# Optimization experiments

Hardware: AMD Instinct MI355X
Metric: run time of the kernel (lower is better)

Reference implementation:

```python
import jax, jax.numpy as jnp
import numpy as np

B, H, W, C = 2, 64, 64, 192
DM = int(2.0 * C)   # d_inner = ssm_ratio * hidden_dim = 384
N = 16              # d_state
R = 12              # dt_rank = ceil(C / 16)
K = 4               # scan directions


def _ln(x, g, b, eps):
    mu = jnp.mean(x, axis=-1, keepdims=True)
    var = jnp.var(x, axis=-1, keepdims=True)
    return (x - mu) * jax.lax.rsqrt(var + eps) * g + b


def setup_inputs() -> dict:
    key = jax.random.key(0)
    ks = jax.random.split(key, 8)
    return {
        "input": jax.random.normal(ks[0], (B, H, W, C), jnp.float32),
        "norm_g": jnp.ones((C,), jnp.float32),
        "norm_b": jnp.zeros((C,), jnp.float32),
        "in_proj_w": jax.random.normal(ks[1], (C, 2 * DM), jnp.float32) * 0.02,
        "conv_w": jax.random.normal(ks[2], (DM, 1, 3, 3), jnp.float32) * 0.1,
        "conv_b": jnp.zeros((DM,), jnp.float32),
        "x_proj_w": jax.random.normal(ks[3], (K, R + 2 * N, DM), jnp.float32) * 0.02,
        "dt_w": jax.random.normal(ks[4], (K, DM, R), jnp.float32) * 0.1,
        "dt_b": jax.random.uniform(ks[5], (K, DM), jnp.float32, -4.0, -2.0),
        "A_logs": jnp.tile(jnp.log(jnp.arange(1, N + 1, dtype=jnp.float32))[None, None, :], (K, DM, 1)),
        "Ds": jnp.ones((K, DM), jnp.float32),
        "out_norm_g": jnp.ones((DM,), jnp.float32),
        "out_norm_b": jnp.zeros((DM,), jnp.float32),
        "out_proj_w": jax.random.normal(ks[6], (DM, C), jnp.float32) * 0.02,
    }


def _selective_scan(us, deltas, A, Bs, Cs):
    # us, deltas: (B,K,D,L); A: (K,D,N); Bs, Cs: (B,K,N,L)
    u_l = jnp.moveaxis(us, -1, 0)       # (L,B,K,D)
    d_l = jnp.moveaxis(deltas, -1, 0)   # (L,B,K,D)
    B_l = jnp.moveaxis(Bs, -1, 0)       # (L,B,K,N)
    C_l = jnp.moveaxis(Cs, -1, 0)       # (L,B,K,N)
    h0 = jnp.zeros(us.shape[:3] + (A.shape[-1],), us.dtype)  # (B,K,D,N)

    def step(h, xs):
        u_t, d_t, b_t, c_t = xs
        dA = jnp.exp(d_t[..., None] * A)                       # (B,K,D,N)
        h = dA * h + (d_t * u_t)[..., None] * b_t[:, :, None, :]
        y = jnp.einsum('bkdn,bkn->bkd', h, c_t)
        return h, y

    _, ys = jax.lax.scan(step, h0, (u_l, d_l, B_l, C_l))
    return jnp.moveaxis(ys, 0, -1)  # (B,K,D,L)


def reference(input, norm_g, norm_b, in_proj_w, conv_w, conv_b, x_proj_w,
              dt_w, dt_b, A_logs, Ds, out_norm_g, out_norm_b, out_proj_w):
    Bz, Hh, Ww, Cc = input.shape
    L = Hh * Ww
    # pre-norm
    xn = _ln(input, norm_g, norm_b, 1e-6)
    # input projection -> x, z
    xz = xn @ in_proj_w                      # (B,H,W,2*DM)
    x, z = jnp.split(xz, 2, axis=-1)
    # depthwise conv + SiLU (channels-first)
    x = jnp.transpose(x, (0, 3, 1, 2))       # (B,DM,H,W)
    Dm = x.shape[1]
    x = jax.lax.conv_general_dilated(
        x, conv_w, (1, 1), 'SAME',
        dimension_numbers=('NCHW', 'OIHW', 'NCHW'),
        feature_group_count=Dm) + conv_b[None, :, None, None]
    x = jax.nn.silu(x)
    # 4-direction cross-scan: hw, wh, and their reverses
    x_flat = x.reshape(Bz, Dm, L)
    x_t = jnp.transpose(x, (0, 1, 3, 2)).reshape(Bz, Dm, L)
    xs = jnp.stack([x_flat, x_t], axis=1)                  # (B,2,DM,L)
    xs = jnp.concatenate([xs, jnp.flip(xs, -1)], axis=1)   # (B,4,DM,L)
    Rr = dt_w.shape[2]
    Nn = A_logs.shape[2]
    x_dbl = jnp.einsum('bkdl,kcd->bkcl', xs, x_proj_w)     # (B,4,R+2N,L)
    dts, Bs, Cs = jnp.split(x_dbl, [Rr, Rr + Nn], axis=2)
    deltas = jax.nn.softplus(
        jnp.einsum('bkrl,kdr->bkdl', dts, dt_w) + dt_b[None, :, :, None])
    A = -jnp.exp(A_logs)                                   # (4,DM,N)
    out_y = _selective_scan(xs, deltas, A, Bs, Cs) + Ds[None, :, :, None] * xs
    # merge the 4 directions back
    inv = jnp.flip(out_y[:, 2:], -1)

    def wh(t):
        return jnp.transpose(t.reshape(Bz, Dm, Ww, Hh), (0, 1, 3, 2)).reshape(Bz, Dm, L)

    y = out_y[:, 0] + inv[:, 0] + wh(out_y[:, 1]) + wh(inv[:, 1])  # (B,DM,L)
    y = jnp.transpose(y, (0, 2, 1))                                # (B,L,DM)
    y = _ln(y, out_norm_g, out_norm_b, 1e-5).reshape(Bz, Hh, Ww, Dm)
    y = y * jax.nn.silu(z)
    out = y @ out_proj_w
    # residual (drop_path=0 -> identity)
    return input + out
```

## Files before the change

kernel.cpp:

```cpp
#include <hip/hip_runtime.h>
#include <hip/hip_bf16.h>
#include <hip/hip_fp16.h>


typedef __attribute__((ext_vector_type(8))) short short8;
typedef __attribute__((ext_vector_type(4))) float floatx4;

__global__ __launch_bounds__(256) void k_ln(const float* __restrict__ in,
                                            const float* __restrict__ g,
                                            const float* __restrict__ be,
                                            __hip_bfloat16* __restrict__ out) {
  int row = blockIdx.x * 4 + (threadIdx.x >> 6);
  int lane = threadIdx.x & 63;
  const float* x = in + (long)row * 192;
  float v0 = x[lane], v1 = x[lane + 64], v2 = x[lane + 128];
  float s = v0 + v1 + v2;
  float s2 = v0 * v0 + v1 * v1 + v2 * v2;
  #pragma unroll
  for (int o = 32; o > 0; o >>= 1) { s += __shfl_xor(s, o); s2 += __shfl_xor(s2, o); }
  float mu = s * (1.f / 192.f);
  float var = s2 * (1.f / 192.f) - mu * mu;
  float r = rsqrtf(var + 1e-6f);
  __hip_bfloat16* op = out + (long)row * 192;
  op[lane]       = __float2bfloat16((v0 - mu) * r * g[lane]       + be[lane]);
  op[lane + 64]  = __float2bfloat16((v1 - mu) * r * g[lane + 64]  + be[lane + 64]);
  op[lane + 128] = __float2bfloat16((v2 - mu) * r * g[lane + 128] + be[lane + 128]);
}

__global__ __launch_bounds__(256) void k_packw(const float* __restrict__ ipw,
                                               const float* __restrict__ xpw,
                                               const float* __restrict__ opw,
                                               __hip_bfloat16* __restrict__ Wt1,
                                               __hip_bfloat16* __restrict__ Wt2,
                                               __hip_bfloat16* __restrict__ Wt3) {
  int idx = blockIdx.x * 256 + threadIdx.x;
  if (idx < 147456) {
    int n = idx / 192, k = idx - n * 192;
    Wt1[idx] = __float2bfloat16(ipw[(long)k * 768 + n]);
  } else if (idx < 147456 + 73728) {
    int t = idx - 147456;
    int j = t / 384;
    float v = (j < 176) ? xpw[t] : 0.f;
    Wt2[t] = __float2bfloat16(v);
  } else if (idx < 147456 + 73728 + 73728) {
    int t = idx - 147456 - 73728;
    int n = t / 384, k = t - n * 384;
    Wt3[t] = __float2bfloat16(opw[(long)k * 192 + n]);
  }
}

__device__ __forceinline__ int inv_dir(int k, int p) {
  int pt = ((p & 63) << 6) | (p >> 6);
  if (k == 0) return p;
  if (k == 1) return pt;
  if (k == 2) return 4095 - p;
  return 4095 - pt;
}
__device__ __forceinline__ int dir_pix(int k, int l) { return inv_dir(k, l); }

template <int EPI>
__global__ __launch_bounds__(256) void k_gemm_mfma(const __hip_bfloat16* __restrict__ A,
                                                   const __hip_bfloat16* __restrict__ Bt,
                                                   const float* __restrict__ Res,
                                                   float* __restrict__ Co,
                                                   __hip_bfloat16* __restrict__ CoB,
                                                   __hip_bfloat16* __restrict__ Co2B,
                                                   float* __restrict__ dtsS,
                                                   float* __restrict__ BCs,
                                                   int M, int N, int Kk) {
  __shared__ __align__(16) short As[64 * 64];
  __shared__ __align__(16) short Bs[64 * 64];
  int tid = threadIdx.x;
  int wave = tid >> 6, lane = tid & 63;
  int mlane = lane & 15, quad = lane >> 4;
  int row0 = blockIdx.y * 64, col0 = blockIdx.x * 64;
  int wr = wave & 1, wc = wave >> 1;
  floatx4 acc[2][2];
  #pragma unroll
  for (int mi = 0; mi < 2; mi++)
    #pragma unroll
    for (int ni = 0; ni < 2; ni++) acc[mi][ni] = (floatx4){0.f, 0.f, 0.f, 0.f};

  for (int k0 = 0; k0 < Kk; k0 += 64) {
    #pragma unroll
    for (int c = tid; c < 512; c += 256) {
      int r = c >> 3, j = c & 7;
      *(float4*)&As[r * 64 + ((j ^ (r & 7)) << 3)] =
          *(const float4*)&A[(long)(row0 + r) * Kk + k0 + j * 8];
    }
    #pragma unroll
    for (int c = tid; c < 512; c += 256) {
      int r = c >> 3, j = c & 7;
      *(float4*)&Bs[r * 64 + ((j ^ (r & 7)) << 3)] =
          *(const float4*)&Bt[(long)(col0 + r) * Kk + k0 + j * 8];
    }
    __syncthreads();
    short8 af[2][2], bf[2][2];
    #pragma unroll
    for (int mi = 0; mi < 2; mi++) {
      int r = wr * 32 + mi * 16 + mlane;
      #pragma unroll
      for (int kk = 0; kk < 2; kk++) {
        int jx = (kk * 4 + quad) ^ (r & 7);
        af[mi][kk] = *(const short8*)&As[r * 64 + jx * 8];
      }
    }
    #pragma unroll
    for (int ni = 0; ni < 2; ni++) {
      int rn = wc * 32 + ni * 16 + mlane;
      #pragma unroll
      for (int kk = 0; kk < 2; kk++) {
        int jx = (kk * 4 + quad) ^ (rn & 7);
        bf[ni][kk] = *(const short8*)&Bs[rn * 64 + jx * 8];
      }
    }
    #pragma unroll
    for (int kk = 0; kk < 2; kk++)
      #pragma unroll
      for (int mi = 0; mi < 2; mi++)
        #pragma unroll
        for (int ni = 0; ni < 2; ni++)
          acc[mi][ni] = __builtin_amdgcn_mfma_f32_16x16x32_bf16(af[mi][kk], bf[ni][kk],
                                                                acc[mi][ni], 0, 0, 0);
    __syncthreads();
  }
  #pragma unroll
  for (int mi = 0; mi < 2; mi++) {
    #pragma unroll
    for (int ni = 0; ni < 2; ni++) {
      int cc = col0 + wc * 32 + ni * 16 + mlane;
      #pragma unroll
      for (int i = 0; i < 4; i++) {
        int rr = row0 + wr * 32 + mi * 16 + quad * 4 + i;
        float v = acc[mi][ni][i];
        if (EPI == 1) {
          Co[(long)rr * N + cc] = v + Res[(long)rr * N + cc];
        } else if (EPI == 2) {
          if (cc < 384) CoB[(long)rr * 384 + cc] = __float2bfloat16(v);
          else          Co2B[(long)rr * 384 + (cc - 384)] = __float2bfloat16(v);
        } else {
          if (cc < 176) {
            int k4 = (cc >= 132) ? 3 : (cc >= 88) ? 2 : (cc >= 44) ? 1 : 0;
            int c = cc - k4 * 44;
            int b = rr >> 12, p = rr & 4095;
            long lbase = ((long)((b << 2) + k4) << 12) + p;
            if (c < 12) dtsS[lbase * 12 + c] = v;
            else        BCs[lbase * 32 + (c - 12)] = v;
          }
        }
      }
    }
  }
}

__global__ __launch_bounds__(384) void k_conv(const __hip_bfloat16* __restrict__ xbufB,
                                              const float* __restrict__ cw,
                                              const float* __restrict__ cb,
                                              __hip_bfloat16* __restrict__ xcb) {
  int row = blockIdx.x;
  int b = row >> 12, p = row & 4095;
  int h = p >> 6, w0 = p & 63;
  int d = threadIdx.x;
  float acc = cb[d];
  const float* wt = cw + d * 9;
  #pragma unroll
  for (int dh = -1; dh <= 1; dh++) {
    int hh = h + dh;
    if (hh < 0 || hh > 63) continue;
    #pragma unroll
    for (int dw = -1; dw <= 1; dw++) {
      int ww = w0 + dw;
      if (ww < 0 || ww > 63) continue;
      acc += __bfloat162float(xbufB[((long)(b << 12) + (hh << 6) + ww) * 384 + d])
             * wt[(dh + 1) * 3 + (dw + 1)];
    }
  }
  float sg = 1.f / (1.f + __expf(-acc));
  xcb[(long)row * 384 + d] = __float2bfloat16(acc * sg);
}

__global__ __launch_bounds__(384) void k_dt(const float* __restrict__ dtsS,
                                            const float* __restrict__ dt_w,
                                            const float* __restrict__ dt_b,
                                            const __hip_bfloat16* __restrict__ xcb,
                                            __half2* __restrict__ dpre) {
  int bid = blockIdx.x;
  int chunk = bid & 127, bk = bid >> 7;
  int k = bk & 3, b = bk >> 2;
  int d = threadIdx.x;
  float w[12];
  const float* dwp = dt_w + ((long)(k * 384) + d) * 12;
  #pragma unroll
  for (int r = 0; r < 12; r++) w[r] = dwp[r];
  float db = dt_b[k * 384 + d];
  long base = ((long)bk << 12) + chunk * 32;
  long pbase = ((long)(b << 12)) + chunk * 32;
  #pragma unroll 4
  for (int t = 0; t < 32; t++) {
    const float4* dq = (const float4*)(dtsS + (base + t) * 12);
    float4 q0 = dq[0], q1 = dq[1], q2 = dq[2];
    float x = db + q0.x * w[0] + q0.y * w[1] + q0.z * w[2] + q0.w * w[3]
                 + q1.x * w[4] + q1.y * w[5] + q1.z * w[6] + q1.w * w[7]
                 + q2.x * w[8] + q2.y * w[9] + q2.z * w[10] + q2.w * w[11];
    float e = __expf(x);
    float delta = (x > 15.f) ? x : __logf(1.f + e);
    float u = __bfloat162float(xcb[(pbase + t) * 384 + d]);
    __half2 o;
    o.x = __float2half(delta * u);
    o.y = __float2half(delta);
    dpre[(base + t) * 384 + d] = o;
  }
}

__device__ __forceinline__ void pow16(float r, float* pws) {
  pws[0] = r;
  #pragma unroll
  for (int n = 1; n < 16; n++) {
    int m = n + 1, c = (m + 1) / 2, f = m - c;
    pws[n] = pws[c - 1] * pws[f - 1];
  }
}

__global__ __launch_bounds__(384) void k_scan0(
    const __half2* __restrict__ dpre, const float* __restrict__ BCs,
    const float* __restrict__ A_logs,
    float* __restrict__ Eb, float* __restrict__ Dend) {
  int bid = blockIdx.x;
  int s = bid & 127, bk = bid >> 7;
  int k = bk & 3;
  int d = threadIdx.x;
  const float* al = A_logs + ((long)(k * 384) + d) * 16;
  bool pw = true;
  float av[16];
  #pragma unroll
  for (int n = 0; n < 16; n++) {
    float a = __expf(al[n]);
    av[n] = -a;
    pw = pw && (fabsf(a - (float)(n + 1)) < 1e-3f);
  }
  float h[16];
  #pragma unroll
  for (int n = 0; n < 16; n++) h[n] = 0.f;
  float cum = 0.f;
  long bpk = (long)bk << 12;

  if (pw) {
    #pragma unroll 4
    for (int t = 0; t < 32; t++) {
      int p = dir_pix(k, s * 32 + t);
      __half2 v = dpre[(bpk + p) * 384 + d];
      float du = __half2float(v.x);
      float delta = __half2float(v.y);
      cum += delta;
      float rr = __expf(-delta);
      float pws[16]; pow16(rr, pws);
      const float4* Bq = (const float4*)(BCs + (bpk + p) * 32);
      float4 b0 = Bq[0], b1 = Bq[1], b2 = Bq[2], b3 = Bq[3];
      float Bl[16] = {b0.x, b0.y, b0.z, b0.w, b1.x, b1.y, b1.z, b1.w,
                      b2.x, b2.y, b2.z, b2.w, b3.x, b3.y, b3.z, b3.w};
      #pragma unroll
      for (int n = 0; n < 16; n++) h[n] = pws[n] * h[n] + du * Bl[n];
    }
  } else {
    for (int t = 0; t < 32; t++) {
      int p = dir_pix(k, s * 32 + t);
      __half2 v = dpre[(bpk + p) * 384 + d];
      float du = __half2float(v.x);
      float delta = __half2float(v.y);
      cum += delta;
      const float4* Bq = (const float4*)(BCs + (bpk + p) * 32);
      float4 b0 = Bq[0], b1 = Bq[1], b2 = Bq[2], b3 = Bq[3];
      float Bl[16] = {b0.x, b0.y, b0.z, b0.w, b1.x, b1.y, b1.z, b1.w,
                      b2.x, b2.y, b2.z, b2.w, b3.x, b3.y, b3.z, b3.w};
      #pragma unroll
      for (int n = 0; n < 16; n++) {
        float dA = __expf(delta * av[n]);
        h[n] = dA * h[n] + du * Bl[n];
      }
    }
  }
  long g = (long)bk * 128 + s;
  float* Ep = Eb + g * 6144 + d * 16;
  #pragma unroll
  for (int n = 0; n < 16; n++) Ep[n] = h[n];
  Dend[g * 384 + d] = cum;
}

__global__ __launch_bounds__(128) void k_combine(float* __restrict__ Eb,
                                                 const float* __restrict__ Dend,
                                                 const float* __restrict__ A_logs) {
  int bid = blockIdx.x;
  int bk = bid / 384;
  int d = bid - bk * 384;
  int k = bk & 3;
  int s = threadIdx.x;
  const float* al = A_logs + ((long)(k * 384) + d) * 16;
  bool pw = true;
  float av[16];
  #pragma unroll
  for (int n = 0; n < 16; n++) {
    float a = __expf(al[n]);
    av[n] = -a;
    pw = pw && (fabsf(a - (float)(n + 1)) < 1e-3f);
  }

  long ebase = ((long)bk * 128 + s) * 6144 + d * 16;
  float e[16];
  *(float4*)&e[0]  = *(const float4*)&Eb[ebase + 0];
  *(float4*)&e[4]  = *(const float4*)&Eb[ebase + 4];
  *(float4*)&e[8]  = *(const float4*)&Eb[ebase + 8];
  *(float4*)&e[12] = *(const float4*)&Eb[ebase + 12];
  float sig = Dend[((long)bk * 128 + s) * 384 + d];

  __shared__ float sE[128][17];
  sE[s][0] = sig;
  #pragma unroll
  for (int n = 0; n < 16; n++) sE[s][1 + n] = e[n];
  __syncthreads();

  for (int o = 1; o < 128; o <<= 1) {
    float ps = 0.f, pe[16];
    bool act = (s >= o);
    if (act) {
      ps = sE[s - o][0];
      #pragma unroll
      for (int n = 0; n < 16; n++) pe[n] = sE[s - o][1 + n];
    }
    __syncthreads();
    if (act) {
      if (pw) {
        float rc = __expf(-sig);
        float pwr[16]; pow16(rc, pwr);
        #pragma unroll
        for (int n = 0; n < 16; n++) e[n] += pwr[n] * pe[n];
      } else {
        #pragma unroll
        for (int n = 0; n < 16; n++) e[n] += __expf(av[n] * sig) * pe[n];
      }
      sig += ps;
      sE[s][0] = sig;
      #pragma unroll
      for (int n = 0; n < 16; n++) sE[s][1 + n] = e[n];
    }
    __syncthreads();
  }

  float ho[16];
  if (s == 0) {
    #pragma unroll
    for (int n = 0; n < 16; n++) ho[n] = 0.f;
  } else {
    #pragma unroll
    for (int n = 0; n < 16; n++) ho[n] = sE[s - 1][1 + n];
  }
  *(float4*)&Eb[ebase + 0]  = *(float4*)&ho[0];
  *(float4*)&Eb[ebase + 4]  = *(float4*)&ho[4];
  *(float4*)&Eb[ebase + 8]  = *(float4*)&ho[8];
  *(float4*)&Eb[ebase + 12] = *(float4*)&ho[12];
}

template <int ATOMIC>
__global__ __launch_bounds__(384) void k_scan1(
    const __half2* __restrict__ dpre, const float* __restrict__ BCs,
    const float* __restrict__ A_logs, const float* __restrict__ Eb,
    __hip_bfloat16* __restrict__ ybufB, float* __restrict__ ysum) {
  int bid = blockIdx.x;
  int s = bid & 127, bk = bid >> 7;
  int k = bk & 3, b = bk >> 2;
  int d = threadIdx.x;
  const float* al = A_logs + ((long)(k * 384) + d) * 16;
  bool pw = true;
  float av[16];
  #pragma unroll
  for (int n = 0; n < 16; n++) {
    float a = __expf(al[n]);
    av[n] = -a;
    pw = pw && (fabsf(a - (float)(n + 1)) < 1e-3f);
  }
  float h[16];
  const float* hp = Eb + ((long)bk * 128 + s) * 6144 + d * 16;
  #pragma unroll
  for (int n = 0; n < 16; n++) h[n] = hp[n];
  long bpk = (long)bk << 12;
  long bpix = (long)(b << 12);

  if (pw) {
    #pragma unroll 4
    for (int t = 0; t < 32; t++) {
      int p = dir_pix(k, s * 32 + t);
      __half2 v = dpre[(bpk + p) * 384 + d];
      float du = __half2float(v.x);
      float delta = __half2float(v.y);
      float rr = __expf(-delta);
      float pws[16]; pow16(rr, pws);
      const float4* Bq = (const float4*)(BCs + (bpk + p) * 32);
      float4 b0 = Bq[0], b1 = Bq[1], b2 = Bq[2], b3 = Bq[3];
      float Bl[16] = {b0.x, b0.y, b0.z, b0.w, b1.x, b1.y, b1.z, b1.w,
                      b2.x, b2.y, b2.z, b2.w, b3.x, b3.y, b3.z, b3.w};
      const float4* Cq = Bq + 4;
      float4 c0 = Cq[0], c1 = Cq[1], c2 = Cq[2], c3 = Cq[3];
      float Cl[16] = {c0.x, c0.y, c0.z, c0.w, c1.x, c1.y, c1.z, c1.w,
                      c2.x, c2.y, c2.z, c2.w, c3.x, c3.y, c3.z, c3.w};
      float y = 0.f;
      #pragma unroll
      for (int n = 0; n < 16; n++) { h[n] = pws[n] * h[n] + du * Bl[n]; y += h[n] * Cl[n]; }
      if (ATOMIC) atomicAdd(&ysum[(bpix + p) * 384 + d], y);
      else        ybufB[(bpk + p) * 384 + d] = __float2bfloat16(y);
    }
  } else {
    for (int t = 0; t < 32; t++) {
      int p = dir_pix(k, s * 32 + t);
      __half2 v = dpre[(bpk + p) * 384 + d];
      float du = __half2float(v.x);
      float delta = __half2float(v.y);
      const float4* Bq = (const float4*)(BCs + (bpk + p) * 32);
      float4 b0 = Bq[0], b1 = Bq[1], b2 = Bq[2], b3 = Bq[3];
      float Bl[16] = {b0.x, b0.y, b0.z, b0.w, b1.x, b1.y, b1.z, b1.w,
                      b2.x, b2.y, b2.z, b2.w, b3.x, b3.y, b3.z, b3.w};
      const float4* Cq = Bq + 4;
      float4 c0 = Cq[0], c1 = Cq[1], c2 = Cq[2], c3 = Cq[3];
      float Cl[16] = {c0.x, c0.y, c0.z, c0.w, c1.x, c1.y, c1.z, c1.w,
                      c2.x, c2.y, c2.z, c2.w, c3.x, c3.y, c3.z, c3.w};
      float y = 0.f;
      #pragma unroll
      for (int n = 0; n < 16; n++) {
        float dA = __expf(delta * av[n]);
        h[n] = dA * h[n] + du * Bl[n];
        y += h[n] * Cl[n];
      }
      if (ATOMIC) atomicAdd(&ysum[(bpix + p) * 384 + d], y);
      else        ybufB[(bpk + p) * 384 + d] = __float2bfloat16(y);
    }
  }
}

template <int GATHER>
__global__ __launch_bounds__(384) void k_merge(const __hip_bfloat16* __restrict__ yinB,
                                               const float* __restrict__ yinF,
                                               const __hip_bfloat16* __restrict__ xcb,
                                               const __hip_bfloat16* __restrict__ zbufB,
                                               const float* __restrict__ Ds,
                                               const float* __restrict__ g,
                                               const float* __restrict__ be,
                                               __hip_bfloat16* __restrict__ yactb) {
  int row = blockIdx.x;
  int d = threadIdx.x;
  float v;
  if (GATHER) {
    int b = row >> 12, p = row & 4095;
    long base = ((long)(b << 2) << 12) + p;
    v = __bfloat162float(yinB[base * 384 + d])
      + __bfloat162float(yinB[(base + 4096) * 384 + d])
      + __bfloat162float(yinB[(base + 8192) * 384 + d])
      + __bfloat162float(yinB[(base + 12288) * 384 + d]);
  } else {
    v = yinF[(long)row * 384 + d];
  }
  float sd = Ds[d] + Ds[384 + d] + Ds[768 + d] + Ds[1152 + d];
  v += __bfloat162float(xcb[(long)row * 384 + d]) * sd;
  float s1 = v, s2 = v * v;
  #pragma unroll
  for (int o = 32; o > 0; o >>= 1) { s1 += __shfl_xor(s1, o); s2 += __shfl_xor(s2, o); }
  __shared__ float r1[6], r2[6];
  int wv = threadIdx.x >> 6;
  if ((threadIdx.x & 63) == 0) { r1[wv] = s1; r2[wv] = s2; }
  __syncthreads();
  float S1 = 0.f, S2 = 0.f;
  #pragma unroll
  for (int i = 0; i < 6; i++) { S1 += r1[i]; S2 += r2[i]; }
  float mu = S1 * (1.f / 384.f);
  float var = S2 * (1.f / 384.f) - mu * mu;
  float rr = rsqrtf(var + 1e-5f);
  float yn = (v - mu) * rr * g[d] + be[d];
  float z = __bfloat162float(zbufB[(long)row * 384 + d]);
  float sg = z / (1.f + __expf(-z));
  yactb[(long)row * 384 + d] = __float2bfloat16(yn * sg);
}

extern "C" void kernel_launch(void* const* d_in, const int* in_sizes, int n_in,
                              void* d_out, int out_size, void* d_ws, size_t ws_size,
                              hipStream_t stream) {
  const float* input      = (const float*)d_in[0];
  const float* norm_g     = (const float*)d_in[1];
  const float* norm_b     = (const float*)d_in[2];
  const float* in_proj_w  = (const float*)d_in[3];
  const float* conv_w     = (const float*)d_in[4];
  const float* conv_b     = (const float*)d_in[5];
  const float* x_proj_w   = (const float*)d_in[6];
  const float* dt_w       = (const float*)d_in[7];
  const float* dt_b       = (const float*)d_in[8];
  const float* A_logs     = (const float*)d_in[9];
  const float* Ds         = (const float*)d_in[10];
  const float* out_norm_g = (const float*)d_in[11];
  const float* out_norm_b = (const float*)d_in[12];
  const float* out_proj_w = (const float*)d_in[13];
  float* out = (float*)d_out;

  bool big = ws_size >= (size_t)34226176 * 4;

  float* ws = (float*)d_ws;
  long o = 0;
  __hip_bfloat16* xnb   = (__hip_bfloat16*)(ws + o); o += 786432;
  __hip_bfloat16* xbufB = (__hip_bfloat16*)(ws + o); o += 1572864;
  __hip_bfloat16* zbufB = (__hip_bfloat16*)(ws + o); o += 1572864;
  __hip_bfloat16* xcb   = (__hip_bfloat16*)(ws + o); o += 1572864;
  __hip_bfloat16* Wt1   = (__hip_bfloat16*)(ws + o); o += 73728;
  __hip_bfloat16* Wt2   = (__hip_bfloat16*)(ws + o); o += 36864;
  __hip_bfloat16* Wt3   = (__hip_bfloat16*)(ws + o); o += 36864;
  float* dtsS           = ws + o;                    o += 393216;
  float* BCs            = ws + o;                    o += 1048576;
  __half2* dpre         = (__half2*)(ws + o);        o += 12582912;
  float* Eb             = ws + o;                    o += 6291456;
  float* Dend           = ws + o;                    o += 393216;
  __hip_bfloat16* ybufB = (__hip_bfloat16*)(ws + o);
  float* ysum           = ws + o;                    o += big ? 6291456 : 3145728;
  __hip_bfloat16* yactb = (__hip_bfloat16*)(ws + o); o += 1572864;

  k_ln<<<dim3(2048), dim3(256), 0, stream>>>(input, norm_g, norm_b, xnb);
  k_packw<<<dim3(1152), dim3(256), 0, stream>>>(in_proj_w, x_proj_w, out_proj_w, Wt1, Wt2, Wt3);
  k_gemm_mfma<2><<<dim3(12, 128), dim3(256), 0, stream>>>(xnb, Wt1, nullptr, nullptr, xbufB, zbufB,
                                                          nullptr, nullptr, 8192, 768, 192);
  k_conv<<<dim3(8192), dim3(384), 0, stream>>>(xbufB, conv_w, conv_b, xcb);
  k_gemm_mfma<3><<<dim3(3, 128), dim3(256), 0, stream>>>(xcb, Wt2, nullptr, nullptr, nullptr, nullptr,
                                                         dtsS, BCs, 8192, 192, 384);
  k_dt<<<dim3(1024), dim3(384), 0, stream>>>(dtsS, dt_w, dt_b, xcb, dpre);
  k_scan0<<<dim3(1024), dim3(384), 0, stream>>>(dpre, BCs, A_logs, Eb, Dend);
  k_combine<<<dim3(3072), dim3(128), 0, stream>>>(Eb, Dend, A_logs);
  if (big) {
    k_scan1<0><<<dim3(1024), dim3(384), 0, stream>>>(dpre, BCs, A_logs, Eb, ybufB, nullptr);
    k_merge<1><<<dim3(8192), dim3(384), 0, stream>>>(ybufB, nullptr, xcb, zbufB, Ds,
                                                     out_norm_g, out_norm_b, yactb);
  } else {
    hipMemsetAsync(ysum, 0, (size_t)3145728 * 4, stream);
    k_scan1<1><<<dim3(1024), dim3(384), 0, stream>>>(dpre, BCs, A_logs, Eb, nullptr, ysum);
    k_merge<0><<<dim3(8192), dim3(384), 0, stream>>>(nullptr, ysum, xcb, zbufB, Ds,
                                                     out_norm_g, out_norm_b, yactb);
  }
  k_gemm_mfma<1><<<dim3(3, 128), dim3(256), 0, stream>>>(yactb, Wt3, input, out, nullptr, nullptr,
                                                         nullptr, nullptr, 8192, 192, 384);
}
```

Before: 260.4 us.

## Shrink dpre to fp16 delta, recompute du in scans, tile conv and in-proj GEMM

k_dt now stores only delta as fp16 instead of a (delta*u, delta) half2 pair, which halves the largest intermediate buffer. Both scan kernels read u from xcb and compute du themselves. The depthwise conv now has each thread produce 4 adjacent pixels from a 3x6 register window, so overlapping input loads are reused. The in-projection GEMM uses a 128-wide N tile, and the lower workspace threshold lets the big path be chosen more often. In exchange the scans do an extra bf16 load per step.

Measured after the change: 244.2 us. 6.3% less time.

```diff
diff --git a/kernel.cpp b/kernel.cpp
--- a/kernel.cpp
+++ b/kernel.cpp
@@ -58,7 +58,7 @@
 }
 __device__ __forceinline__ int dir_pix(int k, int l) { return inv_dir(k, l); }
 
-template <int EPI>
+template <int EPI, int TN>
 __global__ __launch_bounds__(256) void k_gemm_mfma(const __hip_bfloat16* __restrict__ A,
                                                    const __hip_bfloat16* __restrict__ Bt,
                                                    const float* __restrict__ Res,
@@ -68,18 +68,19 @@
                                                    float* __restrict__ dtsS,
                                                    float* __restrict__ BCs,
                                                    int M, int N, int Kk) {
+  constexpr int NI = TN / 32;
   __shared__ __align__(16) short As[64 * 64];
-  __shared__ __align__(16) short Bs[64 * 64];
+  __shared__ __align__(16) short Bs[TN * 64];
   int tid = threadIdx.x;
   int wave = tid >> 6, lane = tid & 63;
   int mlane = lane & 15, quad = lane >> 4;
-  int row0 = blockIdx.y * 64, col0 = blockIdx.x * 64;
+  int row0 = blockIdx.y * 64, col0 = blockIdx.x * TN;
   int wr = wave & 1, wc = wave >> 1;
-  floatx4 acc[2][2];
+  floatx4 acc[2][NI];
   #pragma unroll
   for (int mi = 0; mi < 2; mi++)
     #pragma unroll
-    for (int ni = 0; ni < 2; ni++) acc[mi][ni] = (floatx4){0.f, 0.f, 0.f, 0.f};
+    for (int ni = 0; ni < NI; ni++) acc[mi][ni] = (floatx4){0.f, 0.f, 0.f, 0.f};
 
   for (int k0 = 0; k0 < Kk; k0 += 64) {
     #pragma unroll
@@ -89,13 +90,13 @@
           *(const float4*)&A[(long)(row0 + r) * Kk + k0 + j * 8];
     }
     #pragma unroll
-    for (int c = tid; c < 512; c += 256) {
+    for (int c = tid; c < TN * 8; c += 256) {
       int r = c >> 3, j = c & 7;
       *(float4*)&Bs[r * 64 + ((j ^ (r & 7)) << 3)] =
           *(const float4*)&Bt[(long)(col0 + r) * Kk + k0 + j * 8];
     }
     __syncthreads();
-    short8 af[2][2], bf[2][2];
+    short8 af[2][2], bf[NI][2];
     #pragma unroll
     for (int mi = 0; mi < 2; mi++) {
       int r = wr * 32 + mi * 16 + mlane;
@@ -106,8 +107,8 @@
       }
     }
     #pragma unroll
-    for (int ni = 0; ni < 2; ni++) {
-      int rn = wc * 32 + ni * 16 + mlane;
+    for (int ni = 0; ni < NI; ni++) {
+      int rn = wc * (TN / 2) + ni * 16 + mlane;
       #pragma unroll
       for (int kk = 0; kk < 2; kk++) {
         int jx = (kk * 4 + quad) ^ (rn & 7);
@@ -119,7 +120,7 @@
       #pragma unroll
       for (int mi = 0; mi < 2; mi++)
         #pragma unroll
-        for (int ni = 0; ni < 2; ni++)
+        for (int ni = 0; ni < NI; ni++)
           acc[mi][ni] = __builtin_amdgcn_mfma_f32_16x16x32_bf16(af[mi][kk], bf[ni][kk],
                                                                 acc[mi][ni], 0, 0, 0);
     __syncthreads();
@@ -127,8 +128,8 @@
   #pragma unroll
   for (int mi = 0; mi < 2; mi++) {
     #pragma unroll
-    for (int ni = 0; ni < 2; ni++) {
-      int cc = col0 + wc * 32 + ni * 16 + mlane;
+    for (int ni = 0; ni < NI; ni++) {
+      int cc = col0 + wc * (TN / 2) + ni * 16 + mlane;
       #pragma unroll
       for (int i = 0; i < 4; i++) {
         int rr = row0 + wr * 32 + mi * 16 + quad * 4 + i;
@@ -157,36 +158,47 @@
                                               const float* __restrict__ cw,
                                               const float* __restrict__ cb,
                                               __hip_bfloat16* __restrict__ xcb) {
-  int row = blockIdx.x;
-  int b = row >> 12, p = row & 4095;
-  int h = p >> 6, w0 = p & 63;
+  int blk = blockIdx.x;
+  int wg = blk & 15, h = (blk >> 4) & 63, b = blk >> 10;
+  int w0 = wg * 4;
   int d = threadIdx.x;
-  float acc = cb[d];
-  const float* wt = cw + d * 9;
-  #pragma unroll
-  for (int dh = -1; dh <= 1; dh++) {
-    int hh = h + dh;
-    if (hh < 0 || hh > 63) continue;
-    #pragma unroll
-    for (int dw = -1; dw <= 1; dw++) {
-      int ww = w0 + dw;
-      if (ww < 0 || ww > 63) continue;
-      acc += __bfloat162float(xbufB[((long)(b << 12) + (hh << 6) + ww) * 384 + d])
-             * wt[(dh + 1) * 3 + (dw + 1)];
-    }
-  }
-  float sg = 1.f / (1.f + __expf(-acc));
-  xcb[(long)row * 384 + d] = __float2bfloat16(acc * sg);
+  float wt[9];
+  const float* wp = cw + d * 9;
+  #pragma unroll
+  for (int i = 0; i < 9; i++) wt[i] = wp[i];
+  float bias = cb[d];
+  float v[3][6];
+  #pragma unroll
+  for (int r = 0; r < 3; r++) {
+    int hh = h + r - 1;
+    bool rok = (hh >= 0) && (hh < 64);
+    #pragma unroll
+    for (int c = 0; c < 6; c++) {
+      int ww = w0 + c - 1;
+      bool ok = rok && (ww >= 0) && (ww < 64);
+      v[r][c] = ok ? __bfloat162float(xbufB[((long)(b << 12) + (hh << 6) + ww) * 384 + d]) : 0.f;
+    }
+  }
+  #pragma unroll
+  for (int i = 0; i < 4; i++) {
+    float acc = bias;
+    #pragma unroll
+    for (int r = 0; r < 3; r++)
+      #pragma unroll
+      for (int c = 0; c < 3; c++)
+        acc += v[r][i + c] * wt[r * 3 + c];
+    float sg = 1.f / (1.f + __expf(-acc));
+    xcb[((long)(b << 12) + (h << 6) + (w0 + i)) * 384 + d] = __float2bfloat16(acc * sg);
+  }
 }
 
 __global__ __launch_bounds__(384) void k_dt(const float* __restrict__ dtsS,
                                             const float* __restrict__ dt_w,
                                             const float* __restrict__ dt_b,
-                                            const __hip_bfloat16* __restrict__ xcb,
-                                            __half2* __restrict__ dpre) {
+                                            __half* __restrict__ dpre) {
   int bid = blockIdx.x;
   int chunk = bid & 127, bk = bid >> 7;
-  int k = bk & 3, b = bk >> 2;
+  int k = bk & 3;
   int d = threadIdx.x;
   float w[12];
   const float* dwp = dt_w + ((long)(k * 384) + d) * 12;
@@ -194,7 +206,6 @@
   for (int r = 0; r < 12; r++) w[r] = dwp[r];
   float db = dt_b[k * 384 + d];
   long base = ((long)bk << 12) + chunk * 32;
-  long pbase = ((long)(b << 12)) + chunk * 32;
   #pragma unroll 4
   for (int t = 0; t < 32; t++) {
     const float4* dq = (const float4*)(dtsS + (base + t) * 12);
@@ -204,11 +215,7 @@
                  + q2.x * w[8] + q2.y * w[9] + q2.z * w[10] + q2.w * w[11];
     float e = __expf(x);
     float delta = (x > 15.f) ? x : __logf(1.f + e);
-    float u = __bfloat162float(xcb[(pbase + t) * 384 + d]);
-    __half2 o;
-    o.x = __float2half(delta * u);
-    o.y = __float2half(delta);
-    dpre[(base + t) * 384 + d] = o;
+    dpre[(base + t) * 384 + d] = __float2half(delta);
   }
 }
 
@@ -222,12 +229,13 @@
 }
 
 __global__ __launch_bounds__(384) void k_scan0(
-    const __half2* __restrict__ dpre, const float* __restrict__ BCs,
+    const __half* __restrict__ dpre, const float* __restrict__ BCs,
+    const __hip_bfloat16* __restrict__ xcb,
     const float* __restrict__ A_logs,
     float* __restrict__ Eb, float* __restrict__ Dend) {
   int bid = blockIdx.x;
   int s = bid & 127, bk = bid >> 7;
-  int k = bk & 3;
+  int k = bk & 3, b = bk >> 2;
   int d = threadIdx.x;
   const float* al = A_logs + ((long)(k * 384) + d) * 16;
   bool pw = true;
@@ -243,15 +251,16 @@
   for (int n = 0; n < 16; n++) h[n] = 0.f;
   float cum = 0.f;
   long bpk = (long)bk << 12;
+  long bpix = (long)(b << 12);
 
   if (pw) {
     #pragma unroll 4
     for (int t = 0; t < 32; t++) {
       int p = dir_pix(k, s * 32 + t);
-      __half2 v = dpre[(bpk + p) * 384 + d];
-      float du = __half2float(v.x);
-      float delta = __half2float(v.y);
+      float delta = __half2float(dpre[(bpk + p) * 384 + d]);
+      float u = __bfloat162float(xcb[(bpix + p) * 384 + d]);
       cum += delta;
+      float du = delta * u;
       float rr = __expf(-delta);
       float pws[16]; pow16(rr, pws);
       const float4* Bq = (const float4*)(BCs + (bpk + p) * 32);
@@ -264,10 +273,10 @@
   } else {
     for (int t = 0; t < 32; t++) {
       int p = dir_pix(k, s * 32 + t);
-      __half2 v = dpre[(bpk + p) * 384 + d];
-      float du = __half2float(v.x);
-      float delta = __half2float(v.y);
+      float delta = __half2float(dpre[(bpk + p) * 384 + d]);
+      float u = __bfloat162float(xcb[(bpix + p) * 384 + d]);
       cum += delta;
+      float du = delta * u;
       const float4* Bq = (const float4*)(BCs + (bpk + p) * 32);
       float4 b0 = Bq[0], b1 = Bq[1], b2 = Bq[2], b3 = Bq[3];
       float Bl[16] = {b0.x, b0.y, b0.z, b0.w, b1.x, b1.y, b1.z, b1.w,
@@ -361,7 +370,8 @@
 
 template <int ATOMIC>
 __global__ __launch_bounds__(384) void k_scan1(
-    const __half2* __restrict__ dpre, const float* __restrict__ BCs,
+    const __half* __restrict__ dpre, const float* __restrict__ BCs,
+    const __hip_bfloat16* __restrict__ xcb,
     const float* __restrict__ A_logs, const float* __restrict__ Eb,
     __hip_bfloat16* __restrict__ ybufB, float* __restrict__ ysum) {
   int bid = blockIdx.x;
@@ -388,9 +398,9 @@
     #pragma unroll 4
     for (int t = 0; t < 32; t++) {
       int p = dir_pix(k, s * 32 + t);
-      __half2 v = dpre[(bpk + p) * 384 + d];
-      float du = __half2float(v.x);
-      float delta = __half2float(v.y);
+      float delta = __half2float(dpre[(bpk + p) * 384 + d]);
+      float u = __bfloat162float(xcb[(bpix + p) * 384 + d]);
+      float du = delta * u;
       float rr = __expf(-delta);
       float pws[16]; pow16(rr, pws);
       const float4* Bq = (const float4*)(BCs + (bpk + p) * 32);
@@ -410,9 +420,9 @@
   } else {
     for (int t = 0; t < 32; t++) {
       int p = dir_pix(k, s * 32 + t);
-      __half2 v = dpre[(bpk + p) * 384 + d];
-      float du = __half2float(v.x);
-      float delta = __half2float(v.y);
+      float delta = __half2float(dpre[(bpk + p) * 384 + d]);
+      float u = __bfloat162float(xcb[(bpix + p) * 384 + d]);
+      float du = delta * u;
       const float4* Bq = (const float4*)(BCs + (bpk + p) * 32);
       float4 b0 = Bq[0], b1 = Bq[1], b2 = Bq[2], b3 = Bq[3];
       float Bl[16] = {b0.x, b0.y, b0.z, b0.w, b1.x, b1.y, b1.z, b1.w,
@@ -496,7 +506,7 @@
   const float* out_proj_w = (const float*)d_in[13];
   float* out = (float*)d_out;
 
-  bool big = ws_size >= (size_t)34226176 * 4;
+  bool big = ws_size >= (size_t)27934720 * 4;
 
   float* ws = (float*)d_ws;
   long o = 0;
@@ -509,7 +519,7 @@
   __hip_bfloat16* Wt3   = (__hip_bfloat16*)(ws + o); o += 36864;
   float* dtsS           = ws + o;                    o += 393216;
   float* BCs            = ws + o;                    o += 1048576;
-  __half2* dpre         = (__half2*)(ws + o);        o += 12582912;
+  __half* dpre          = (__half*)(ws + o);         o += 6291456;
   float* Eb             = ws + o;                    o += 6291456;
   float* Dend           = ws + o;                    o += 393216;
   __hip_bfloat16* ybufB = (__hip_bfloat16*)(ws + o);
@@ -518,24 +528,24 @@
 
   k_ln<<<dim3(2048), dim3(256), 0, stream>>>(input, norm_g, norm_b, xnb);
   k_packw<<<dim3(1152), dim3(256), 0, stream>>>(in_proj_w, x_proj_w, out_proj_w, Wt1, Wt2, Wt3);
-  k_gemm_mfma<2><<<dim3(12, 128), dim3(256), 0, stream>>>(xnb, Wt1, nullptr, nullptr, xbufB, zbufB,
-                                                          nullptr, nullptr, 8192, 768, 192);
-  k_conv<<<dim3(8192), dim3(384), 0, stream>>>(xbufB, conv_w, conv_b, xcb);
-  k_gemm_mfma<3><<<dim3(3, 128), dim3(256), 0, stream>>>(xcb, Wt2, nullptr, nullptr, nullptr, nullptr,
-                                                         dtsS, BCs, 8192, 192, 384);
-  k_dt<<<dim3(1024), dim3(384), 0, stream>>>(dtsS, dt_w, dt_b, xcb, dpre);
-  k_scan0<<<dim3(1024), dim3(384), 0, stream>>>(dpre, BCs, A_logs, Eb, Dend);
+  k_gemm_mfma<2, 128><<<dim3(6, 128), dim3(256), 0, stream>>>(xnb, Wt1, nullptr, nullptr, xbufB, zbufB,
+                                                              nullptr, nullptr, 8192, 768, 192);
+  k_conv<<<dim3(2048), dim3(384), 0, stream>>>(xbufB, conv_w, conv_b, xcb);
+  k_gemm_mfma<3, 64><<<dim3(3, 128), dim3(256), 0, stream>>>(xcb, Wt2, nullptr, nullptr, nullptr, nullptr,
+                                                             dtsS, BCs, 8192, 192, 384);
+  k_dt<<<dim3(1024), dim3(384), 0, stream>>>(dtsS, dt_w, dt_b, dpre);
+  k_scan0<<<dim3(1024), dim3(384), 0, stream>>>(dpre, BCs, xcb, A_logs, Eb, Dend);
   k_combine<<<dim3(3072), dim3(128), 0, stream>>>(Eb, Dend, A_logs);
   if (big) {
-    k_scan1<0><<<dim3(1024), dim3(384), 0, stream>>>(dpre, BCs, A_logs, Eb, ybufB, nullptr);
+    k_scan1<0><<<dim3(1024), dim3(384), 0, stream>>>(dpre, BCs, xcb, A_logs, Eb, ybufB, nullptr);
     k_merge<1><<<dim3(8192), dim3(384), 0, stream>>>(ybufB, nullptr, xcb, zbufB, Ds,
                                                      out_norm_g, out_norm_b, yactb);
   } else {
     hipMemsetAsync(ysum, 0, (size_t)3145728 * 4, stream);
-    k_scan1<1><<<dim3(1024), dim3(384), 0, stream>>>(dpre, BCs, A_logs, Eb, nullptr, ysum);
+    k_scan1<1><<<dim3(1024), dim3(384), 0, stream>>>(dpre, BCs, xcb, A_logs, Eb, nullptr, ysum);
     k_merge<0><<<dim3(8192), dim3(384), 0, stream>>>(nullptr, ysum, xcb, zbufB, Ds,
                                                      out_norm_g, out_norm_b, yactb);
   }
-  k_gemm_mfma<1><<<dim3(3, 128), dim3(256), 0, stream>>>(yactb, Wt3, input, out, nullptr, nullptr,
-                                                         nullptr, nullptr, 8192, 192, 384);
-}
+  k_gemm_mfma<1, 64><<<dim3(3, 128), dim3(256), 0, stream>>>(yactb, Wt3, input, out, nullptr, nullptr,
+                                                             nullptr, nullptr, 8192, 192, 384);
+}
```
